# Kernel tuning notes

Measured on AMD Instinct MI355X. Metric: run time of the kernel, lower is better.

Reference implementation:

```python
import jax, jax.numpy as jnp
import numpy as np

D = 8
W = 256
NUM_FREQS = 10
NUM_FREQS_VIEWS = 4
SKIPS = (4,)
PE_DIM = 3 + 2 * 3 * NUM_FREQS        # 63
VE_DIM = 3 + 2 * 3 * NUM_FREQS_VIEWS  # 27
N_RAYS, N_SAMPLES = 4096, 64


def embed(x, num_freqs):
    # torch order: [x, sin(x*f0), cos(x*f0), sin(x*f1), cos(x*f1), ...]
    freqs = (2.0 ** jnp.arange(num_freqs)).astype(x.dtype)
    xf = x[..., None, :] * freqs[:, None]              # [..., F, 3]
    sc = jnp.stack([jnp.sin(xf), jnp.cos(xf)], axis=-2)  # [..., F, 2, 3]
    return jnp.concatenate([x, sc.reshape(*x.shape[:-1], num_freqs * 6)], -1)


def setup_inputs() -> dict:
    key = jax.random.key(0)
    ks = iter(jax.random.split(key, 32))
    inp = {}
    inp["input_pts"] = jax.random.normal(next(ks), (N_RAYS, N_SAMPLES, 3), jnp.float32)
    inp["input_views"] = jax.random.normal(next(ks), (N_RAYS, 3), jnp.float32)
    # pts MLP: layer 5 (index 5) takes W + PE_DIM due to skip after layer 4
    in_dims = [PE_DIM] + [(W + PE_DIM) if i in SKIPS else W for i in range(D - 1)]
    for i, d in enumerate(in_dims):
        inp[f"pts_w{i}"] = jax.random.normal(next(ks), (d, W), jnp.float32) / np.sqrt(d).astype(np.float32)
        inp[f"pts_b{i}"] = jnp.zeros((W,), jnp.float32)
    inp["views_w"] = jax.random.normal(next(ks), (VE_DIM + W, W // 2), jnp.float32) / np.sqrt(VE_DIM + W).astype(np.float32)
    inp["views_b"] = jnp.zeros((W // 2,), jnp.float32)
    inp["feat_w"] = jax.random.normal(next(ks), (W, W), jnp.float32) / np.sqrt(W).astype(np.float32)
    inp["feat_b"] = jnp.zeros((W,), jnp.float32)
    inp["alpha_w"] = jax.random.normal(next(ks), (W, 1), jnp.float32) / np.sqrt(W).astype(np.float32)
    inp["alpha_b"] = jnp.zeros((1,), jnp.float32)
    inp["rgb_w"] = jax.random.normal(next(ks), (W // 2, 3), jnp.float32) / np.sqrt(W // 2).astype(np.float32)
    inp["rgb_b"] = jnp.zeros((3,), jnp.float32)
    return inp


def reference(input_pts, input_views,
              pts_w0, pts_b0, pts_w1, pts_b1, pts_w2, pts_b2, pts_w3, pts_b3,
              pts_w4, pts_b4, pts_w5, pts_b5, pts_w6, pts_b6, pts_w7, pts_b7,
              views_w, views_b, feat_w, feat_b, alpha_w, alpha_b, rgb_w, rgb_b):
    pts_ws = [pts_w0, pts_w1, pts_w2, pts_w3, pts_w4, pts_w5, pts_w6, pts_w7]
    pts_bs = [pts_b0, pts_b1, pts_b2, pts_b3, pts_b4, pts_b5, pts_b6, pts_b7]
    R, S = input_pts.shape[0], input_pts.shape[1]
    ep = embed(input_pts, NUM_FREQS).reshape(-1, PE_DIM)            # [R*S, 63]
    ev = embed(input_views, NUM_FREQS_VIEWS)                        # [R, 27]
    ev = jnp.broadcast_to(ev[:, None, :], (R, S, VE_DIM)).reshape(-1, VE_DIM)
    h = ep
    for i in range(D):
        h = jax.nn.relu(h @ pts_ws[i] + pts_bs[i])
        if i in SKIPS:
            h = jnp.concatenate([ep, h], -1)
    alpha = h @ alpha_w + alpha_b                                    # [R*S, 1]
    feature = h @ feat_w + feat_b                                    # [R*S, W]
    h2 = jax.nn.relu(jnp.concatenate([feature, ev], -1) @ views_w + views_b)
    rgb = h2 @ rgb_w + rgb_b                                         # [R*S, 3]
    return jnp.concatenate([rgb, alpha], -1).reshape(R, S, 4)
```

## Files before the change

### kernel.cpp

```cpp
#include <hip/hip_runtime.h>

typedef _Float16 h16;
typedef __attribute__((ext_vector_type(8))) _Float16 half8;
typedef __attribute__((ext_vector_type(4))) _Float16 half4;
typedef __attribute__((ext_vector_type(4))) float f32x4;

#define LDH 264
#define LDE 72

constexpr size_t OFF_P0 = 0;
constexpr size_t OFF_P1 = 16384;
constexpr size_t OFF_P2 = 81920;
constexpr size_t OFF_P3 = 147456;
constexpr size_t OFF_P4 = 212992;
constexpr size_t OFF_P5 = 278528;
constexpr size_t OFF_P6 = 360448;
constexpr size_t OFF_P7 = 425984;
constexpr size_t OFF_FEAT = 491520;
constexpr size_t OFF_VIEWS = 557056;

__device__ __forceinline__ f32x4 mfma16(half8 a, half8 b, f32x4 c) {
  return __builtin_amdgcn_mfma_f32_16x16x32_f16(a, b, c, 0, 0, 0);
}

__global__ void convw_kernel(const float* __restrict__ src, h16* __restrict__ dst,
                             int Ksrc, int N, int Kp, int p, int npad) {
  int t = blockIdx.x * 256 + threadIdx.x;
  int nfrags = (Kp >> 5) * (N >> 4);
  int frag = t >> 6;
  if (frag >= nfrags) return;
  int l = t & 63;
  int ntiles = N >> 4;
  int kt = frag / ntiles;
  int nt = frag - kt * ntiles;
  int col = nt * 16 + (l & 15);
  int kbase = kt * 32 + (l >> 4) * 8;
  half8 v;
#pragma unroll
  for (int j = 0; j < 8; ++j) {
    int k = kbase + j;
    float x = 0.f;
    if (k < p) {
      x = src[(size_t)k * N + col];
    } else if (k >= p + npad) {
      int r = k - npad;
      if (r < Ksrc) x = src[(size_t)r * N + col];
    }
    v[j] = (h16)x;
  }
  *(half8*)(dst + (size_t)frag * 512 + (size_t)l * 8) = v;
}

struct Params {
  const float* pts;
  const float* views;
  const h16* wf;
  const float* pb[8];
  const float* views_b;
  const float* feat_b;
  const float* alpha_w;
  const float* alpha_b;
  const float* rgb_w;
  const float* rgb_b;
  float* out;
};

template <int KT, int KT0, bool RELU, bool PRE_BAR>
__device__ __forceinline__ void gemm256(const h16* __restrict__ src0, int ld0,
                                        const h16* __restrict__ src1, int ld1,
                                        const h16* __restrict__ wf,
                                        const float* __restrict__ bias,
                                        h16* __restrict__ dst,
                                        int w, int lrow, int lgrp, int l) {
  f32x4 acc[4][4];
  const f32x4 z = {0.f, 0.f, 0.f, 0.f};
#pragma unroll
  for (int mt = 0; mt < 4; ++mt)
#pragma unroll
    for (int nt = 0; nt < 4; ++nt) acc[mt][nt] = z;

#pragma unroll
  for (int kt = 0; kt < KT; ++kt) {
    half8 a[4];
#pragma unroll
    for (int mt = 0; mt < 4; ++mt) {
      const h16* ap;
      if (kt < KT0) ap = src0 + (size_t)(mt * 16 + lrow) * ld0 + kt * 32 + lgrp * 8;
      else          ap = src1 + (size_t)(mt * 16 + lrow) * ld1 + (kt - KT0) * 32 + lgrp * 8;
      a[mt] = *(const half8*)ap;
    }
    half8 b[4];
#pragma unroll
    for (int nt = 0; nt < 4; ++nt)
      b[nt] = *(const half8*)(wf + ((size_t)(kt * 16 + w * 4 + nt) * 64 + l) * 8);
#pragma unroll
    for (int mt = 0; mt < 4; ++mt)
#pragma unroll
      for (int nt = 0; nt < 4; ++nt)
        acc[mt][nt] = mfma16(b[nt], a[mt], acc[mt][nt]);
  }
  if (PRE_BAR) __syncthreads();
#pragma unroll
  for (int mt = 0; mt < 4; ++mt) {
    int row = mt * 16 + lrow;
#pragma unroll
    for (int nt = 0; nt < 4; ++nt) {
      int col0 = w * 64 + nt * 16 + lgrp * 4;
      f32x4 bv = *(const f32x4*)(bias + col0);
      half4 pk;
#pragma unroll
      for (int i = 0; i < 4; ++i) {
        float v = acc[mt][nt][i] + bv[i];
        if (RELU) v = fmaxf(v, 0.f);
        pk[i] = (h16)v;
      }
      *(half4*)(dst + (size_t)row * LDH + col0) = pk;
    }
  }
  __syncthreads();
}

__device__ __forceinline__ void gemm128(const h16* __restrict__ feat,
                                        const h16* __restrict__ evp,
                                        const h16* __restrict__ wf,
                                        const float* __restrict__ bias,
                                        h16* __restrict__ dst,
                                        int w, int lrow, int lgrp, int l) {
  f32x4 acc[4][2];
  const f32x4 z = {0.f, 0.f, 0.f, 0.f};
#pragma unroll
  for (int mt = 0; mt < 4; ++mt) { acc[mt][0] = z; acc[mt][1] = z; }

#pragma unroll
  for (int kt = 0; kt < 9; ++kt) {
    half8 a[4];
    if (kt < 8) {
#pragma unroll
      for (int mt = 0; mt < 4; ++mt)
        a[mt] = *(const half8*)(feat + (size_t)(mt * 16 + lrow) * LDH + kt * 32 + lgrp * 8);
    } else {
      half8 av = *(const half8*)(evp + lgrp * 8);
#pragma unroll
      for (int mt = 0; mt < 4; ++mt) a[mt] = av;
    }
    half8 b[2];
#pragma unroll
    for (int nt = 0; nt < 2; ++nt)
      b[nt] = *(const half8*)(wf + ((size_t)(kt * 8 + w * 2 + nt) * 64 + l) * 8);
#pragma unroll
    for (int mt = 0; mt < 4; ++mt)
#pragma unroll
      for (int nt = 0; nt < 2; ++nt)
        acc[mt][nt] = mfma16(b[nt], a[mt], acc[mt][nt]);
  }
  __syncthreads();
#pragma unroll
  for (int mt = 0; mt < 4; ++mt) {
    int row = mt * 16 + lrow;
#pragma unroll
    for (int nt = 0; nt < 2; ++nt) {
      int col0 = w * 32 + nt * 16 + lgrp * 4;
      f32x4 bv = *(const f32x4*)(bias + col0);
      half4 pk;
#pragma unroll
      for (int i = 0; i < 4; ++i)
        pk[i] = (h16)fmaxf(acc[mt][nt][i] + bv[i], 0.f);
      *(half4*)(dst + (size_t)row * LDH + col0) = pk;
    }
  }
  __syncthreads();
}

__global__ __launch_bounds__(256, 2) void nerf_kernel(Params P) {
  __shared__ __align__(16) h16 ep[64 * LDE];
  __shared__ __align__(16) h16 h[64 * LDH];
  __shared__ __align__(16) h16 evp[32];
  __shared__ float alpha_s[64];

  const int tid = threadIdx.x;
  const int w = tid >> 6, l = tid & 63;
  const int lrow = l & 15, lgrp = l >> 4;
  const int ray = blockIdx.x;

  if (tid < 64) {
    const int s = tid;
    const float x0 = P.pts[((size_t)ray * 64 + s) * 3 + 0];
    const float x1 = P.pts[((size_t)ray * 64 + s) * 3 + 1];
    const float x2 = P.pts[((size_t)ray * 64 + s) * 3 + 2];
    h16* e = ep + (size_t)s * LDE;
    e[0] = (h16)x0; e[1] = (h16)x1; e[2] = (h16)x2;
#pragma unroll
    for (int f = 0; f < 10; ++f) {
      const float sc = (float)(1 << f);
      e[3 + 6 * f + 0] = (h16)sinf(x0 * sc);
      e[3 + 6 * f + 1] = (h16)sinf(x1 * sc);
      e[3 + 6 * f + 2] = (h16)sinf(x2 * sc);
      e[3 + 6 * f + 3] = (h16)cosf(x0 * sc);
      e[3 + 6 * f + 4] = (h16)cosf(x1 * sc);
      e[3 + 6 * f + 5] = (h16)cosf(x2 * sc);
    }
    e[63] = (h16)0.f;
  } else if (tid < 96) {
    const int idx = tid - 64;
    float v = 0.f;
    if (idx < 27) {
      if (idx < 3) {
        v = P.views[(size_t)ray * 3 + idx];
      } else {
        const int f = (idx - 3) / 6, rem = (idx - 3) % 6, d = rem % 3;
        const float x = P.views[(size_t)ray * 3 + d] * (float)(1 << f);
        v = (rem < 3) ? sinf(x) : cosf(x);
      }
    }
    evp[idx] = (h16)v;
  }
  __syncthreads();

  gemm256<2, 2, true, false>(ep, LDE, ep, LDE, P.wf + OFF_P0, P.pb[0], h, w, lrow, lgrp, l);
  gemm256<8, 0, true, true>(ep, LDE, h, LDH, P.wf + OFF_P1, P.pb[1], h, w, lrow, lgrp, l);
  gemm256<8, 0, true, true>(ep, LDE, h, LDH, P.wf + OFF_P2, P.pb[2], h, w, lrow, lgrp, l);
  gemm256<8, 0, true, true>(ep, LDE, h, LDH, P.wf + OFF_P3, P.pb[3], h, w, lrow, lgrp, l);
  gemm256<8, 0, true, true>(ep, LDE, h, LDH, P.wf + OFF_P4, P.pb[4], h, w, lrow, lgrp, l);
  gemm256<10, 2, true, true>(ep, LDE, h, LDH, P.wf + OFF_P5, P.pb[5], h, w, lrow, lgrp, l);
  gemm256<8, 0, true, true>(ep, LDE, h, LDH, P.wf + OFF_P6, P.pb[6], h, w, lrow, lgrp, l);
  gemm256<8, 0, true, true>(ep, LDE, h, LDH, P.wf + OFF_P7, P.pb[7], h, w, lrow, lgrp, l);

  {
    const int s = tid >> 2, q = tid & 3;
    float sum = 0.f;
#pragma unroll 8
    for (int k = 0; k < 64; ++k)
      sum += (float)h[(size_t)s * LDH + q * 64 + k] * P.alpha_w[q * 64 + k];
    sum += __shfl_xor(sum, 1);
    sum += __shfl_xor(sum, 2);
    if (q == 0) alpha_s[s] = sum + P.alpha_b[0];
  }

  gemm256<8, 0, false, true>(ep, LDE, h, LDH, P.wf + OFF_FEAT, P.feat_b, h, w, lrow, lgrp, l);

  gemm128(h, evp, P.wf + OFF_VIEWS, P.views_b, h, w, lrow, lgrp, l);

  {
    const int s = tid >> 2, q = tid & 3;
    float r0 = 0.f, r1 = 0.f, r2 = 0.f;
#pragma unroll 8
    for (int k = 0; k < 32; ++k) {
      const int kk = q * 32 + k;
      const float hv = (float)h[(size_t)s * LDH + kk];
      r0 += hv * P.rgb_w[kk * 3 + 0];
      r1 += hv * P.rgb_w[kk * 3 + 1];
      r2 += hv * P.rgb_w[kk * 3 + 2];
    }
    r0 += __shfl_xor(r0, 1); r0 += __shfl_xor(r0, 2);
    r1 += __shfl_xor(r1, 1); r1 += __shfl_xor(r1, 2);
    r2 += __shfl_xor(r2, 1); r2 += __shfl_xor(r2, 2);
    if (q == 0) {
      float4 o;
      o.x = r0 + P.rgb_b[0];
      o.y = r1 + P.rgb_b[1];
      o.z = r2 + P.rgb_b[2];
      o.w = alpha_s[s];
      *(float4*)(P.out + ((size_t)ray * 64 + s) * 4) = o;
    }
  }
}

extern "C" void kernel_launch(void* const* d_in, const int* in_sizes, int n_in,
                              void* d_out, int out_size, void* d_ws, size_t ws_size,
                              hipStream_t stream) {
  h16* wsw = (h16*)d_ws;
  auto conv = [&](int idx, int Ksrc, int N, int Kp, int p, int npad, size_t off) {
    int nfrags = (Kp / 32) * (N / 16);
    int total = nfrags * 64;
    convw_kernel<<<(total + 255) / 256, 256, 0, stream>>>(
        (const float*)d_in[idx], wsw + off, Ksrc, N, Kp, p, npad);
  };
  conv(2, 63, 256, 64, 63, 1, OFF_P0);
  conv(4, 256, 256, 256, 256, 0, OFF_P1);
  conv(6, 256, 256, 256, 256, 0, OFF_P2);
  conv(8, 256, 256, 256, 256, 0, OFF_P3);
  conv(10, 256, 256, 256, 256, 0, OFF_P4);
  conv(12, 319, 256, 320, 63, 1, OFF_P5);
  conv(14, 256, 256, 256, 256, 0, OFF_P6);
  conv(16, 256, 256, 256, 256, 0, OFF_P7);
  conv(20, 256, 256, 256, 256, 0, OFF_FEAT);
  conv(18, 283, 128, 288, 283, 5, OFF_VIEWS);

  Params P;
  P.pts = (const float*)d_in[0];
  P.views = (const float*)d_in[1];
  P.wf = wsw;
  for (int i = 0; i < 8; ++i) P.pb[i] = (const float*)d_in[3 + 2 * i];
  P.views_b = (const float*)d_in[19];
  P.feat_b = (const float*)d_in[21];
  P.alpha_w = (const float*)d_in[22];
  P.alpha_b = (const float*)d_in[23];
  P.rgb_w = (const float*)d_in[24];
  P.rgb_b = (const float*)d_in[25];
  P.out = (float*)d_out;

  nerf_kernel<<<4096, 256, 0, stream>>>(P);
}
```

Measured before the change: 383.1 us.

## Switch MLP GEMMs to 32x32x16 MFMA with eight waves per block

Replaces the 16x16x32 MFMA tiling with 32x32x16 MFMA. The weight-fragment packing in the conversion kernel is changed to match, and blocks grow to 512 threads, with each of 8 waves computing a 32-column slice for all 64 samples. The views layer is inlined and runs on 4 of the 8 waves. The aim is to issue fewer matrix instructions and to hide latency with more waves per block. In exchange, launch bounds of 512x4 tighten the register budget, which could cause spills, and LDS use may limit how many blocks fit on a CU.

```diff
diff --git a/kernel.cpp b/kernel.cpp
--- a/kernel.cpp
+++ b/kernel.cpp
@@ -4,6 +4,7 @@
 typedef __attribute__((ext_vector_type(8))) _Float16 half8;
 typedef __attribute__((ext_vector_type(4))) _Float16 half4;
 typedef __attribute__((ext_vector_type(4))) float f32x4;
+typedef __attribute__((ext_vector_type(16))) float f32x16;
 
 #define LDH 264
 #define LDE 72
@@ -19,22 +20,22 @@
 constexpr size_t OFF_FEAT = 491520;
 constexpr size_t OFF_VIEWS = 557056;
 
-__device__ __forceinline__ f32x4 mfma16(half8 a, half8 b, f32x4 c) {
-  return __builtin_amdgcn_mfma_f32_16x16x32_f16(a, b, c, 0, 0, 0);
+__device__ __forceinline__ f32x16 mfma32(half8 a, half8 b, f32x16 c) {
+  return __builtin_amdgcn_mfma_f32_32x32x16_f16(a, b, c, 0, 0, 0);
 }
 
 __global__ void convw_kernel(const float* __restrict__ src, h16* __restrict__ dst,
                              int Ksrc, int N, int Kp, int p, int npad) {
   int t = blockIdx.x * 256 + threadIdx.x;
-  int nfrags = (Kp >> 5) * (N >> 4);
+  int nfrags = (Kp >> 4) * (N >> 5);
   int frag = t >> 6;
   if (frag >= nfrags) return;
   int l = t & 63;
-  int ntiles = N >> 4;
+  int ntiles = N >> 5;
   int kt = frag / ntiles;
   int nt = frag - kt * ntiles;
-  int col = nt * 16 + (l & 15);
-  int kbase = kt * 32 + (l >> 4) * 8;
+  int col = nt * 32 + (l & 31);
+  int kbase = kt * 16 + (l >> 5) * 8;
   half8 v;
 #pragma unroll
   for (int j = 0; j < 8; ++j) {
@@ -71,107 +72,50 @@
                                         const h16* __restrict__ wf,
                                         const float* __restrict__ bias,
                                         h16* __restrict__ dst,
-                                        int w, int lrow, int lgrp, int l) {
-  f32x4 acc[4][4];
-  const f32x4 z = {0.f, 0.f, 0.f, 0.f};
-#pragma unroll
-  for (int mt = 0; mt < 4; ++mt)
-#pragma unroll
-    for (int nt = 0; nt < 4; ++nt) acc[mt][nt] = z;
+                                        int w, int l) {
+  const int lr = l & 31;
+  const int lk = (l >> 5) * 8;
+  f32x16 acc[2];
+  acc[0] = (f32x16)0.f;
+  acc[1] = (f32x16)0.f;
 
 #pragma unroll
   for (int kt = 0; kt < KT; ++kt) {
-    half8 a[4];
-#pragma unroll
-    for (int mt = 0; mt < 4; ++mt) {
+    half8 a[2];
+#pragma unroll
+    for (int mt = 0; mt < 2; ++mt) {
       const h16* ap;
-      if (kt < KT0) ap = src0 + (size_t)(mt * 16 + lrow) * ld0 + kt * 32 + lgrp * 8;
-      else          ap = src1 + (size_t)(mt * 16 + lrow) * ld1 + (kt - KT0) * 32 + lgrp * 8;
+      if (kt < KT0) ap = src0 + (size_t)(mt * 32 + lr) * ld0 + kt * 16 + lk;
+      else          ap = src1 + (size_t)(mt * 32 + lr) * ld1 + (kt - KT0) * 16 + lk;
       a[mt] = *(const half8*)ap;
     }
-    half8 b[4];
-#pragma unroll
-    for (int nt = 0; nt < 4; ++nt)
-      b[nt] = *(const half8*)(wf + ((size_t)(kt * 16 + w * 4 + nt) * 64 + l) * 8);
-#pragma unroll
-    for (int mt = 0; mt < 4; ++mt)
-#pragma unroll
-      for (int nt = 0; nt < 4; ++nt)
-        acc[mt][nt] = mfma16(b[nt], a[mt], acc[mt][nt]);
+    half8 b = *(const half8*)(wf + ((size_t)(kt * 8 + w) * 64 + l) * 8);
+#pragma unroll
+    for (int mt = 0; mt < 2; ++mt)
+      acc[mt] = mfma32(b, a[mt], acc[mt]);
   }
   if (PRE_BAR) __syncthreads();
 #pragma unroll
-  for (int mt = 0; mt < 4; ++mt) {
-    int row = mt * 16 + lrow;
-#pragma unroll
-    for (int nt = 0; nt < 4; ++nt) {
-      int col0 = w * 64 + nt * 16 + lgrp * 4;
-      f32x4 bv = *(const f32x4*)(bias + col0);
+  for (int mt = 0; mt < 2; ++mt) {
+    int row = mt * 32 + lr;
+#pragma unroll
+    for (int g = 0; g < 4; ++g) {
+      int n0 = w * 32 + g * 8 + (l >> 5) * 4;
+      f32x4 bv = *(const f32x4*)(bias + n0);
       half4 pk;
 #pragma unroll
       for (int i = 0; i < 4; ++i) {
-        float v = acc[mt][nt][i] + bv[i];
+        float v = acc[mt][g * 4 + i] + bv[i];
         if (RELU) v = fmaxf(v, 0.f);
         pk[i] = (h16)v;
       }
-      *(half4*)(dst + (size_t)row * LDH + col0) = pk;
+      *(half4*)(dst + (size_t)row * LDH + n0) = pk;
     }
   }
   __syncthreads();
 }
 
-__device__ __forceinline__ void gemm128(const h16* __restrict__ feat,
-                                        const h16* __restrict__ evp,
-                                        const h16* __restrict__ wf,
-                                        const float* __restrict__ bias,
-                                        h16* __restrict__ dst,
-                                        int w, int lrow, int lgrp, int l) {
-  f32x4 acc[4][2];
-  const f32x4 z = {0.f, 0.f, 0.f, 0.f};
-#pragma unroll
-  for (int mt = 0; mt < 4; ++mt) { acc[mt][0] = z; acc[mt][1] = z; }
-
-#pragma unroll
-  for (int kt = 0; kt < 9; ++kt) {
-    half8 a[4];
-    if (kt < 8) {
-#pragma unroll
-      for (int mt = 0; mt < 4; ++mt)
-        a[mt] = *(const half8*)(feat + (size_t)(mt * 16 + lrow) * LDH + kt * 32 + lgrp * 8);
-    } else {
-      half8 av = *(const half8*)(evp + lgrp * 8);
-#pragma unroll
-      for (int mt = 0; mt < 4; ++mt) a[mt] = av;
-    }
-    half8 b[2];
-#pragma unroll
-    for (int nt = 0; nt < 2; ++nt)
-      b[nt] = *(const half8*)(wf + ((size_t)(kt * 8 + w * 2 + nt) * 64 + l) * 8);
-#pragma unroll
-    for (int mt = 0; mt < 4; ++mt)
-#pragma unroll
-      for (int nt = 0; nt < 2; ++nt)
-        acc[mt][nt] = mfma16(b[nt], a[mt], acc[mt][nt]);
-  }
-  __syncthreads();
-#pragma unroll
-  for (int mt = 0; mt < 4; ++mt) {
-    int row = mt * 16 + lrow;
-#pragma unroll
-    for (int nt = 0; nt < 2; ++nt) {
-      int col0 = w * 32 + nt * 16 + lgrp * 4;
-      f32x4 bv = *(const f32x4*)(bias + col0);
-      half4 pk;
-#pragma unroll
-      for (int i = 0; i < 4; ++i)
-        pk[i] = (h16)fmaxf(acc[mt][nt][i] + bv[i], 0.f);
-      *(half4*)(dst + (size_t)row * LDH + col0) = pk;
-    }
-  }
-  __syncthreads();
-}
-
-__global__ __launch_bounds__(256, 2) void nerf_kernel(Params P) {
+__global__ __launch_bounds__(512, 4) void nerf_kernel(Params P) {
   __shared__ __align__(16) h16 ep[64 * LDE];
   __shared__ __align__(16) h16 h[64 * LDH];
   __shared__ __align__(16) h16 evp[32];
@@ -179,7 +123,8 @@
 
   const int tid = threadIdx.x;
   const int w = tid >> 6, l = tid & 63;
-  const int lrow = l & 15, lgrp = l >> 4;
+  const int lr = l & 31;
+  const int lk = (l >> 5) * 8;
   const int ray = blockIdx.x;
 
   if (tid < 64) {
@@ -216,16 +161,16 @@
   }
   __syncthreads();
 
-  gemm256<2, 2, true, false>(ep, LDE, ep, LDE, P.wf + OFF_P0, P.pb[0], h, w, lrow, lgrp, l);
-  gemm256<8, 0, true, true>(ep, LDE, h, LDH, P.wf + OFF_P1, P.pb[1], h, w, lrow, lgrp, l);
-  gemm256<8, 0, true, true>(ep, LDE, h, LDH, P.wf + OFF_P2, P.pb[2], h, w, lrow, lgrp, l);
-  gemm256<8, 0, true, true>(ep, LDE, h, LDH, P.wf + OFF_P3, P.pb[3], h, w, lrow, lgrp, l);
-  gemm256<8, 0, true, true>(ep, LDE, h, LDH, P.wf + OFF_P4, P.pb[4], h, w, lrow, lgrp, l);
-  gemm256<10, 2, true, true>(ep, LDE, h, LDH, P.wf + OFF_P5, P.pb[5], h, w, lrow, lgrp, l);
-  gemm256<8, 0, true, true>(ep, LDE, h, LDH, P.wf + OFF_P6, P.pb[6], h, w, lrow, lgrp, l);
-  gemm256<8, 0, true, true>(ep, LDE, h, LDH, P.wf + OFF_P7, P.pb[7], h, w, lrow, lgrp, l);
-
-  {
+  gemm256<4, 4, true, false>(ep, LDE, ep, LDE, P.wf + OFF_P0, P.pb[0], h, w, l);
+  gemm256<16, 0, true, true>(ep, LDE, h, LDH, P.wf + OFF_P1, P.pb[1], h, w, l);
+  gemm256<16, 0, true, true>(ep, LDE, h, LDH, P.wf + OFF_P2, P.pb[2], h, w, l);
+  gemm256<16, 0, true, true>(ep, LDE, h, LDH, P.wf + OFF_P3, P.pb[3], h, w, l);
+  gemm256<16, 0, true, true>(ep, LDE, h, LDH, P.wf + OFF_P4, P.pb[4], h, w, l);
+  gemm256<20, 4, true, true>(ep, LDE, h, LDH, P.wf + OFF_P5, P.pb[5], h, w, l);
+  gemm256<16, 0, true, true>(ep, LDE, h, LDH, P.wf + OFF_P6, P.pb[6], h, w, l);
+  gemm256<16, 0, true, true>(ep, LDE, h, LDH, P.wf + OFF_P7, P.pb[7], h, w, l);
+
+  if (tid < 256) {
     const int s = tid >> 2, q = tid & 3;
     float sum = 0.f;
 #pragma unroll 8
@@ -236,11 +181,51 @@
     if (q == 0) alpha_s[s] = sum + P.alpha_b[0];
   }
 
-  gemm256<8, 0, false, true>(ep, LDE, h, LDH, P.wf + OFF_FEAT, P.feat_b, h, w, lrow, lgrp, l);
-
-  gemm128(h, evp, P.wf + OFF_VIEWS, P.views_b, h, w, lrow, lgrp, l);
+  gemm256<16, 0, false, true>(ep, LDE, h, LDH, P.wf + OFF_FEAT, P.feat_b, h, w, l);
 
   {
+    f32x16 acc[2];
+    acc[0] = (f32x16)0.f;
+    acc[1] = (f32x16)0.f;
+    if (w < 4) {
+#pragma unroll
+      for (int kt = 0; kt < 18; ++kt) {
+        half8 a[2];
+        if (kt < 16) {
+#pragma unroll
+          for (int mt = 0; mt < 2; ++mt)
+            a[mt] = *(const half8*)(h + (size_t)(mt * 32 + lr) * LDH + kt * 16 + lk);
+        } else {
+          half8 av = *(const half8*)(evp + (kt - 16) * 16 + lk);
+          a[0] = av; a[1] = av;
+        }
+        half8 b = *(const half8*)(P.wf + OFF_VIEWS + ((size_t)(kt * 4 + w) * 64 + l) * 8);
+#pragma unroll
+        for (int mt = 0; mt < 2; ++mt)
+          acc[mt] = mfma32(b, a[mt], acc[mt]);
+      }
+    }
+    __syncthreads();
+    if (w < 4) {
+#pragma unroll
+      for (int mt = 0; mt < 2; ++mt) {
+        int row = mt * 32 + lr;
+#pragma unroll
+        for (int g = 0; g < 4; ++g) {
+          int n0 = w * 32 + g * 8 + (l >> 5) * 4;
+          f32x4 bv = *(const f32x4*)(P.views_b + n0);
+          half4 pk;
+#pragma unroll
+          for (int i = 0; i < 4; ++i)
+            pk[i] = (h16)fmaxf(acc[mt][g * 4 + i] + bv[i], 0.f);
+          *(half4*)(h + (size_t)row * LDH + n0) = pk;
+        }
+      }
+    }
+    __syncthreads();
+  }
+
+  if (tid < 256) {
     const int s = tid >> 2, q = tid & 3;
     float r0 = 0.f, r1 = 0.f, r2 = 0.f;
 #pragma unroll 8
@@ -270,7 +255,7 @@
                               hipStream_t stream) {
   h16* wsw = (h16*)d_ws;
   auto conv = [&](int idx, int Ksrc, int N, int Kp, int p, int npad, size_t off) {
-    int nfrags = (Kp / 32) * (N / 16);
+    int nfrags = (Kp / 16) * (N / 32);
     int total = nfrags * 64;
     convw_kernel<<<(total + 255) / 256, 256, 0, stream>>>(
         (const float*)d_in[idx], wsw + off, Ksrc, N, Kp, p, npad);
@@ -299,5 +284,5 @@
   P.rgb_b = (const float*)d_in[25];
   P.out = (float*)d_out;
 
-  nerf_kernel<<<4096, 256, 0, stream>>>(P);
-}
+  nerf_kernel<<<4096, 512, 0, stream>>>(P);
+}
```

Measured after the change: 383.4 us. Within noise of the previous version (+0.1%).
